# Optimization experiments

Hardware: AMD Instinct MI355X
Metric: run time of the kernel (lower is better)

Reference implementation:

```python
import jax, jax.numpy as jnp
import numpy as np

HEADS = 8
OUT_CH = 128
DIMH_V = 16      # out_channels // heads
DIMH_QK = 8      # dim_head_v // 2
DIM = 128        # attention axis length == init dim
QKV_CH = 256     # heads * (dim_head_v + 2*dim_head_qk) == 2*out_channels
F_QR, F_KR, F_SV, F_SVE = 0.3, 0.3, 0.5, 0.3
BN_EPS = 1e-5


def _bn(x, gamma, beta, axes):
    # BatchNorm in training mode: per-channel (axis=1) batch statistics.
    mean = jnp.mean(x, axis=axes, keepdims=True)
    var = jnp.var(x, axis=axes, keepdims=True)
    xhat = (x - mean) * jax.lax.rsqrt(var + BN_EPS)
    shape = [1] * x.ndim
    shape[1] = -1
    return xhat * gamma.reshape(shape) + beta.reshape(shape)


def setup_inputs() -> dict:
    key = jax.random.key(0)
    ks = jax.random.split(key, 3)
    x = jax.random.normal(ks[0], (8, 128, 64, 128), dtype=jnp.float32)
    w_qkv = jax.random.normal(ks[1], (QKV_CH, 128), dtype=jnp.float32) * 0.05
    relative = jax.random.normal(ks[2], (2 * DIMH_V, 2 * DIM - 1), dtype=jnp.float32) * np.sqrt(1.0 / DIMH_V)
    ones = lambda c: jnp.ones((c,), jnp.float32)
    zeros = lambda c: jnp.zeros((c,), jnp.float32)
    return {
        "x": x, "w_qkv": w_qkv,
        "g1": ones(QKV_CH), "b1": zeros(QKV_CH),
        "g2": ones(QKV_CH), "b2": zeros(QKV_CH),
        "gs": ones(3 * HEADS), "bs": zeros(3 * HEADS),
        "go": ones(2 * OUT_CH), "bo": zeros(2 * OUT_CH),
        "relative": relative,
    }


def reference(x, w_qkv, g1, b1, g2, b2, gs, bs, go, bo, relative):
    N, C, Wax, H = x.shape  # flag=True: permute (0,2,1,3)
    xb = jnp.transpose(x, (0, 2, 1, 3)).reshape(N * Wax, C, H)

    # conv1x1 (no bias) + BN, then bn_qkv
    qkv = jnp.einsum('bch,oc->boh', xb, w_qkv)
    qkv = _bn(qkv, g1, b1, (0, 2))
    qkv = _bn(qkv, g2, b2, (0, 2))

    qkv = qkv.reshape(N * Wax, HEADS, 2 * DIMH_V, H)
    q = qkv[:, :, :DIMH_QK]                      # [b,g,8,H]
    k = qkv[:, :, DIMH_QK:2 * DIMH_QK]           # [b,g,8,H]
    v = qkv[:, :, 2 * DIMH_QK:]                  # [b,g,16,H]

    # gather relative embeddings: index[i,j] = i - j + H - 1
    idx = jnp.arange(H)[:, None] - jnp.arange(H)[None, :] + H - 1
    emb = relative[:, idx]                       # [32,H,H]
    q_emb = emb[:DIMH_QK]
    k_emb = emb[DIMH_QK:2 * DIMH_QK]
    v_emb = emb[2 * DIMH_QK:]

    qr = jnp.einsum('bgci,cij->bgij', q, q_emb) * F_QR
    kr = jnp.swapaxes(jnp.einsum('bgci,cij->bgij', k, k_emb), 2, 3) * F_KR
    qk = jnp.einsum('bgci,bgcj->bgij', q, k)

    stacked = jnp.concatenate([qk, qr, kr], axis=1)           # [b,3g,H,H]
    stacked = _bn(stacked, gs, bs, (0, 2, 3))
    stacked = stacked.reshape(N * Wax, 3, HEADS, H, H).sum(axis=1)
    sim = jax.nn.softmax(stacked, axis=3)                     # [b,g,H,H]

    sv = jnp.einsum('bgij,bgcj->bgci', sim, v) * F_SV
    sve = jnp.einsum('bgij,cij->bgci', sim, v_emb) * F_SVE
    so = jnp.concatenate([sv, sve], axis=-1).reshape(N * Wax, 2 * OUT_CH, H)
    so = _bn(so, go, bo, (0, 2))

    out = so.reshape(N, Wax, OUT_CH, 2, H).sum(axis=3)        # [N,W,Cout,H]
    return jnp.transpose(out, (0, 2, 1, 3))                   # flag=True
```

## Files before the change

### kernel.cpp

```cpp
#include <hip/hip_runtime.h>
#include <hip/hip_fp16.h>
#include <math.h>

#define B_TOT 512
#define CQKV  256
#define CIN   128
#define HLEN  128

static constexpr float F_QR = 0.3f, F_KR = 0.3f, F_SV = 0.5f, F_SVE = 0.3f;
static constexpr float EPS = 1e-5f;

typedef __attribute__((ext_vector_type(8))) short short8v;
typedef __attribute__((ext_vector_type(8))) _Float16 half8v;
typedef __attribute__((ext_vector_type(2))) _Float16 half2v;
typedef __attribute__((ext_vector_type(4))) float float4v;

#if __has_builtin(__builtin_amdgcn_fdot2)
#define HAVE_FDOT2 1
#endif

__device__ __forceinline__ unsigned short f2bf(float f) {
    unsigned u = __float_as_uint(f);
    unsigned r = u + 0x7fffu + ((u >> 16) & 1u);
    return (unsigned short)(r >> 16);
}
__device__ __forceinline__ unsigned short f2h(float f) {
    return __half_as_ushort(__float2half(f));
}

__global__ __launch_bounds__(256, 3) void k_qkv(const float* __restrict__ x,
                                                const float* __restrict__ w,
                                                float* __restrict__ qkv,
                                                double* __restrict__ accA) {
    __shared__ unsigned short As[64][136];
    __shared__ unsigned short Xs[256][64];
    __shared__ float wsum[64][2];
    int bid = blockIdx.x;
    int n   = bid >> 7;
    int sub = bid & 127;
    int mt  = sub >> 2;
    int ot  = sub & 3;
    int m0  = mt << 8;
    int o0  = ot << 6;
    int t   = threadIdx.x;

    if (t < 64) { wsum[t][0] = 0.f; wsum[t][1] = 0.f; }

#pragma unroll
    for (int it = 0; it < 8; ++it) {
        int idx = it * 256 + t;
        int o = idx >> 5, c4 = (idx & 31) << 2;
        float4 wv = *(const float4*)(w + (size_t)(o0 + o) * CIN + c4);
        As[o][c4 + 0] = f2bf(wv.x);
        As[o][c4 + 1] = f2bf(wv.y);
        As[o][c4 + 2] = f2bf(wv.z);
        As[o][c4 + 3] = f2bf(wv.w);
    }

    const float* xn = x + (size_t)n * CIN * 8192 + m0;

    int wv_ = t >> 6, l = t & 63;
    int lr = l & 15, lh = l >> 4;
    int mw = wv_ << 6;

    float4v acc[4][4];
#pragma unroll
    for (int a = 0; a < 4; ++a)
#pragma unroll
        for (int b2 = 0; b2 < 4; ++b2) acc[a][b2] = (float4v){0.f, 0.f, 0.f, 0.f};

    for (int s = 0; s < 2; ++s) {
        int c0 = s << 6;
        __syncthreads();
#pragma unroll
        for (int it = 0; it < 16; ++it) {
            int c  = (it << 2) + (t >> 6);
            int m4 = (t & 63) << 2;
            float4 xv = *(const float4*)(xn + (size_t)(c0 + c) * 8192 + m4);
            float vals[4] = {xv.x, xv.y, xv.z, xv.w};
#pragma unroll
            for (int j = 0; j < 4; ++j) {
                int m = m4 + j;
                int cs = (((c >> 3) ^ ((m >> 2) & 7)) << 3) | (c & 7);
                Xs[m][cs] = f2bf(vals[j]);
            }
        }
        __syncthreads();
#pragma unroll
        for (int ks = 0; ks < 2; ++ks) {
            short8v af[4], bf[4];
#pragma unroll
            for (int a = 0; a < 4; ++a)
                af[a] = *(const short8v*)&As[a * 16 + lr][c0 + ks * 32 + lh * 8];
#pragma unroll
            for (int b2 = 0; b2 < 4; ++b2) {
                int m  = mw + b2 * 16 + lr;
                int cb = (ks * 4 + lh) ^ ((m >> 2) & 7);
                bf[b2] = *(const short8v*)&Xs[m][cb << 3];
            }
#pragma unroll
            for (int a = 0; a < 4; ++a)
#pragma unroll
                for (int b2 = 0; b2 < 4; ++b2)
                    acc[a][b2] = __builtin_amdgcn_mfma_f32_16x16x32_bf16(
                        af[a], bf[b2], acc[a][b2], 0, 0, 0);
        }
    }

#pragma unroll
    for (int a = 0; a < 4; ++a) {
#pragma unroll
        for (int b2 = 0; b2 < 4; ++b2) {
            int m  = m0 + mw + b2 * 16 + lr;
            int bb = n * 64 + (m >> 7);
            int h  = m & 127;
#pragma unroll
            for (int r = 0; r < 4; ++r) {
                int o = o0 + a * 16 + lh * 4 + r;
                qkv[((size_t)bb * CQKV + o) * HLEN + h] = acc[a][b2][r];
            }
        }
    }

#pragma unroll
    for (int a = 0; a < 4; ++a) {
#pragma unroll
        for (int r = 0; r < 4; ++r) {
            float s = 0.f, ss = 0.f;
#pragma unroll
            for (int b2 = 0; b2 < 4; ++b2) {
                float v = acc[a][b2][r];
                s += v; ss += v * v;
            }
#pragma unroll
            for (int off = 1; off < 16; off <<= 1) {
                s  += __shfl_xor(s, off);
                ss += __shfl_xor(ss, off);
            }
            if (lr == 0) {
                int ol = a * 16 + lh * 4 + r;
                atomicAdd(&wsum[ol][0], s);
                atomicAdd(&wsum[ol][1], ss);
            }
        }
    }
    __syncthreads();
    if (t < 64) {
        atomicAdd(&accA[(size_t)(o0 + t) * 2 + 0], (double)wsum[t][0]);
        atomicAdd(&accA[(size_t)(o0 + t) * 2 + 1], (double)wsum[t][1]);
    }
}

__global__ void k_finA(const double* __restrict__ accA,
                       const float* __restrict__ g1, const float* __restrict__ g2,
                       const float* __restrict__ b2,
                       float* __restrict__ scaleA, float* __restrict__ shiftA) {
    int o = threadIdx.x;
    double cnt  = 65536.0;
    double mean = accA[o * 2] / cnt;
    double var  = accA[o * 2 + 1] / cnt - mean * mean;
    float r1 = rsqrtf((float)var + EPS);
    float v2 = g1[o] * g1[o] * (float)var * r1 * r1;
    float sc = g1[o] * g2[o] * r1 * rsqrtf(v2 + EPS);
    scaleA[o] = sc;
    shiftA[o] = b2[o] - (float)mean * sc;
}

__global__ void k_finF(const double* __restrict__ accF,
                       const float* __restrict__ go, const float* __restrict__ bo,
                       float* __restrict__ scaleF, float* __restrict__ shiftF) {
    int o = threadIdx.x;
    double cnt  = 65536.0;
    double mean = accF[o * 2] / cnt;
    double var  = accF[o * 2 + 1] / cnt - mean * mean;
    float sc = go[o] * rsqrtf((float)var + EPS);
    scaleF[o] = sc;
    shiftF[o] = bo[o] - (float)mean * sc;
}

__global__ __launch_bounds__(128) void k_tables(const float* __restrict__ rel,
                                                float* __restrict__ Rq, float* __restrict__ Rk,
                                                float* __restrict__ TqT, float* __restrict__ TkT) {
    int bid = blockIdx.x;
    int i = threadIdx.x;
    int p = bid & 63;
    int c = p >> 3, c2 = p & 7;
    const float* ra = (bid < 64) ? (rel + c * 255)  : (rel + (8 + c) * 255);
    const float* rb = (bid < 64) ? (rel + c2 * 255) : (rel + (8 + c2) * 255);
    float tacc = 0.f;
    for (int kk = 0; kk < 128; ++kk) tacc = fmaf(ra[i + kk], rb[i + kk], tacc);
    if (bid < 64) TqT[i * 64 + p] = tacc; else TkT[i * 64 + p] = tacc;
    if (c2 == 0) {
        float racc = 0.f;
        for (int kk = 0; kk < 128; ++kk) racc += ra[i + kk];
        if (bid < 64) Rq[c * 128 + i] = racc; else Rk[c * 128 + i] = racc;
    }
}

__global__ __launch_bounds__(256) void k_gram(const float* __restrict__ qkv,
                                              const float* __restrict__ scaleA,
                                              const float* __restrict__ shiftA,
                                              const float* __restrict__ Rq,
                                              const float* __restrict__ Rk,
                                              const float* __restrict__ TqT,
                                              const float* __restrict__ TkT,
                                              double* __restrict__ accS) {
    __shared__ float qs[8][132], ks[8][132];
    __shared__ float redA[4][64][4];
    __shared__ float redB[2][18];
    __shared__ float redC[3];
    int blk = blockIdx.x, b = blk >> 3, g = blk & 7;
    int t = threadIdx.x;
    for (int idx = t; idx < 2048; idx += 256) {
        int cc = idx >> 7, h = idx & 127, o = g * 32 + cc;
        float v = qkv[((size_t)b * CQKV + o) * HLEN + h] * scaleA[o] + shiftA[o];
        if (cc < 8) qs[cc][h] = v; else ks[cc - 8][h] = v;
    }
    __syncthreads();
    int lane = t & 63, wv = t >> 6;
    int c = lane >> 3, c2 = lane & 7;
    float gq = 0, gk = 0, tq = 0, tk = 0;
#pragma unroll 4
    for (int ii = 0; ii < 32; ++ii) {
        int i = wv * 32 + ii;
        float a = qs[c][i] * qs[c2][i];
        float e = ks[c][i] * ks[c2][i];
        gq += a; gk += e;
        tq = fmaf(a, TqT[i * 64 + lane], tq);
        tk = fmaf(e, TkT[i * 64 + lane], tk);
    }
    redA[wv][lane][0] = gq; redA[wv][lane][1] = gk;
    redA[wv][lane][2] = tq; redA[wv][lane][3] = tk;

    if (t < 128) {
        int h = t;
        float sqr = 0, skr = 0;
        float sq8l[8], sk8l[8];
#pragma unroll
        for (int c3 = 0; c3 < 8; ++c3) {
            float q0 = qs[c3][h], k0 = ks[c3][h];
            sq8l[c3] = q0; sk8l[c3] = k0;
            sqr = fmaf(q0, Rq[c3 * 128 + h], sqr);
            skr = fmaf(k0, Rk[c3 * 128 + h], skr);
        }
#pragma unroll
        for (int off = 1; off < 64; off <<= 1) {
            sqr += __shfl_xor(sqr, off);
            skr += __shfl_xor(skr, off);
#pragma unroll
            for (int c3 = 0; c3 < 8; ++c3) {
                sq8l[c3] += __shfl_xor(sq8l[c3], off);
                sk8l[c3] += __shfl_xor(sk8l[c3], off);
            }
        }
        if (lane == 0) {
            redB[wv][0] = sqr; redB[wv][1] = skr;
#pragma unroll
            for (int c3 = 0; c3 < 8; ++c3) {
                redB[wv][2 + c3]  = sq8l[c3];
                redB[wv][10 + c3] = sk8l[c3];
            }
        }
    }
    __syncthreads();
    if (t < 64) {
        float Gq = redA[0][t][0] + redA[1][t][0] + redA[2][t][0] + redA[3][t][0];
        float Gk = redA[0][t][1] + redA[1][t][1] + redA[2][t][1] + redA[3][t][1];
        float Tq = redA[0][t][2] + redA[1][t][2] + redA[2][t][2] + redA[3][t][2];
        float Tk = redA[0][t][3] + redA[1][t][3] + redA[2][t][3] + redA[3][t][3];
        float ssqk = Gq * Gk;
#pragma unroll
        for (int off = 1; off < 64; off <<= 1) {
            ssqk += __shfl_xor(ssqk, off);
            Tq   += __shfl_xor(Tq, off);
            Tk   += __shfl_xor(Tk, off);
        }
        if (t == 0) { redC[0] = ssqk; redC[1] = Tq; redC[2] = Tk; }
    }
    __syncthreads();
    if (t == 0) {
        float sqr = redB[0][0] + redB[1][0];
        float skr = redB[0][1] + redB[1][1];
        float sqk = 0;
#pragma unroll
        for (int c3 = 0; c3 < 8; ++c3)
            sqk += (redB[0][2 + c3] + redB[1][2 + c3]) * (redB[0][10 + c3] + redB[1][10 + c3]);
        atomicAdd(&accS[g * 2 + 0], (double)sqk);
        atomicAdd(&accS[g * 2 + 1], (double)redC[0]);
        atomicAdd(&accS[(8 + g) * 2 + 0], (double)(F_QR * sqr));
        atomicAdd(&accS[(8 + g) * 2 + 1], (double)(F_QR * F_QR * redC[1]));
        atomicAdd(&accS[(16 + g) * 2 + 0], (double)(F_KR * skr));
        atomicAdd(&accS[(16 + g) * 2 + 1], (double)(F_KR * F_KR * redC[2]));
    }
}

__global__ void k_sfin(const double* __restrict__ accS,
                       const float* __restrict__ gs, const float* __restrict__ bs,
                       float* __restrict__ scaleS, float* __restrict__ shiftS) {
    int c = threadIdx.x;
    if (c < 24) {
        double cnt  = 512.0 * 128.0 * 128.0;
        double mean = accS[c * 2] / cnt;
        double var  = accS[c * 2 + 1] / cnt - mean * mean;
        float sc = gs[c] * rsqrtf((float)var + EPS);
        scaleS[c] = sc;
        shiftS[c] = bs[c] - (float)mean * sc;
    }
}

__global__ __launch_bounds__(256, 2) void k_attn(const float* __restrict__ qkv,
                                                 const float* __restrict__ scaleA,
                                                 const float* __restrict__ shiftA,
                                                 const float* __restrict__ rel,
                                                 const float* __restrict__ scaleS,
                                                 const float* __restrict__ shiftS,
                                                 float* __restrict__ so,
                                                 double* __restrict__ accF) {
    __shared__ unsigned short qT[128][8];
    __shared__ unsigned short kF[128][8];
    __shared__ unsigned short vB[16][136];
    __shared__ unsigned short rqT[255][8];
    __shared__ unsigned short rkT[255][8];
    __shared__ unsigned short rvA[255][8];
    __shared__ unsigned short rvB[255][8];
    __shared__ unsigned short Pl[128][136];
    __shared__ float accL[32][2];
    int blk = blockIdx.x, b = blk >> 3, g = blk & 7;
    int t = threadIdx.x;
    if (t < 32) { accL[t][0] = 0.f; accL[t][1] = 0.f; }

#pragma unroll
    for (int it = 0; it < 4; ++it) {
        int idx = it * 256 + t;
        int cc = idx >> 5;
        int h4 = (idx & 31) << 2;
        int o = g * 32 + cc;
        float4 v4 = *(const float4*)(qkv + ((size_t)b * CQKV + o) * HLEN + h4);
        float sc = scaleA[o], sh = shiftA[o];
        float f0 = fmaf(v4.x, sc, sh), f1 = fmaf(v4.y, sc, sh);
        float f2 = fmaf(v4.z, sc, sh), f3 = fmaf(v4.w, sc, sh);
        if (cc < 8) {
            qT[h4][cc] = f2h(f0); qT[h4 + 1][cc] = f2h(f1);
            qT[h4 + 2][cc] = f2h(f2); qT[h4 + 3][cc] = f2h(f3);
        } else if (cc < 16) {
            kF[h4][cc - 8] = f2h(f0); kF[h4 + 1][cc - 8] = f2h(f1);
            kF[h4 + 2][cc - 8] = f2h(f2); kF[h4 + 3][cc - 8] = f2h(f3);
        } else {
            uint2 pk;
            pk.x = (unsigned)f2h(f0) | ((unsigned)f2h(f1) << 16);
            pk.y = (unsigned)f2h(f2) | ((unsigned)f2h(f3) << 16);
            *(uint2*)&vB[cc - 16][h4] = pk;
        }
    }
#pragma unroll
    for (int it = 0; it < 8; ++it) {
        int idx = it * 256 + t;
        if (idx < 2040) {
            float4 v = *(const float4*)(rel + (size_t)idx * 4);
            float vv[4] = {v.x, v.y, v.z, v.w};
#pragma unroll
            for (int e = 0; e < 4; ++e) {
                int lin = idx * 4 + e;
                int r = lin / 255;
                int d = lin - r * 255;
                unsigned short us = f2h(vv[e]);
                if (r < 8)       rqT[d][r] = us;
                else if (r < 16) rkT[d][r - 8] = us;
                else if (r < 24) rvA[d][r - 16] = us;
                else             rvB[d][r - 24] = us;
            }
        }
    }
    __syncthreads();

    float cA = scaleS[g], cB = F_QR * scaleS[8 + g], cC = F_KR * scaleS[16 + g];
    float shsum = shiftS[g] + shiftS[8 + g] + shiftS[16 + g];

    int i = t >> 1, j0 = (t & 1) << 6;
    half2v q2[4];
    {
        uint4 qv = *(const uint4*)&qT[i][0];
        q2[0] = *(half2v*)&qv.x; q2[1] = *(half2v*)&qv.y;
        q2[2] = *(half2v*)&qv.z; q2[3] = *(half2v*)&qv.w;
    }

    float p[64];
    float rowmax = -1e30f;
#pragma unroll
    for (int jj = 0; jj < 64; ++jj) {
        int j = j0 + jj;
        uint4 kv = *(const uint4*)&kF[j][0];
        uint4 rq = *(const uint4*)&rqT[i - j + 127][0];
        uint4 rk = *(const uint4*)&rkT[j - i + 127][0];
        half2v* k2p  = (half2v*)&kv;
        half2v* rq2p = (half2v*)&rq;
        half2v* rk2p = (half2v*)&rk;
#ifdef HAVE_FDOT2
        float qk = __builtin_amdgcn_fdot2(q2[0], k2p[0],
                   __builtin_amdgcn_fdot2(q2[1], k2p[1],
                   __builtin_amdgcn_fdot2(q2[2], k2p[2],
                   __builtin_amdgcn_fdot2(q2[3], k2p[3], 0.f, false), false), false), false);
        float qr = __builtin_amdgcn_fdot2(q2[0], rq2p[0],
                   __builtin_amdgcn_fdot2(q2[1], rq2p[1],
                   __builtin_amdgcn_fdot2(q2[2], rq2p[2],
                   __builtin_amdgcn_fdot2(q2[3], rq2p[3], 0.f, false), false), false), false);
        float kr = __builtin_amdgcn_fdot2(k2p[0], rk2p[0],
                   __builtin_amdgcn_fdot2(k2p[1], rk2p[1],
                   __builtin_amdgcn_fdot2(k2p[2], rk2p[2],
                   __builtin_amdgcn_fdot2(k2p[3], rk2p[3], 0.f, false), false), false), false);
#else
        __half2* k2  = (__half2*)&kv;
        __half2* rq2 = (__half2*)&rq;
        __half2* rk2 = (__half2*)&rk;
        __half2* qh2 = (__half2*)&q2[0];
        __half2 hqk = __hfma2(qh2[0], k2[0], __hfma2(qh2[1], k2[1],
                      __hfma2(qh2[2], k2[2], __hmul2(qh2[3], k2[3]))));
        __half2 hqr = __hfma2(qh2[0], rq2[0], __hfma2(qh2[1], rq2[1],
                      __hfma2(qh2[2], rq2[2], __hmul2(qh2[3], rq2[3]))));
        __half2 hkr = __hfma2(k2[0], rk2[0], __hfma2(k2[1], rk2[1],
                      __hfma2(k2[2], rk2[2], __hmul2(k2[3], rk2[3]))));
        float qk = __low2float(hqk) + __high2float(hqk);
        float qr = __low2float(hqr) + __high2float(hqr);
        float kr = __low2float(hkr) + __high2float(hkr);
#endif
        float s = fmaf(qk, cA, fmaf(qr, cB, fmaf(kr, cC, shsum)));
        p[jj] = s;
        rowmax = fmaxf(rowmax, s);
    }
    rowmax = fmaxf(rowmax, __shfl_xor(rowmax, 1));
    float rsum = 0.f;
#pragma unroll
    for (int jj = 0; jj < 64; ++jj) {
        float e = __expf(p[jj] - rowmax);
        p[jj] = e;
        rsum += e;
    }
    rsum += __shfl_xor(rsum, 1);
    float rn = 1.f / rsum;

#pragma unroll
    for (int k8 = 0; k8 < 8; ++k8) {
        uint4 w4;
        unsigned* wp = (unsigned*)&w4;
#pragma unroll
        for (int e = 0; e < 4; ++e) {
            __half2 h2 = __floats2half2_rn(p[8 * k8 + 2 * e] * rn,
                                           p[8 * k8 + 2 * e + 1] * rn);
            wp[e] = *(unsigned*)&h2;
        }
        *(uint4*)&Pl[i][j0 + 8 * k8] = w4;
    }

    __half2 acc2[8];
#pragma unroll
    for (int m = 0; m < 8; ++m) acc2[m] = __floats2half2_rn(0.f, 0.f);
#pragma unroll
    for (int jj = 0; jj < 64; ++jj) {
        int j = j0 + jj;
        int d = i - j + 127;
        __half2 p2 = __float2half2_rn(p[jj]);
        uint4 ra = *(const uint4*)&rvA[d][0];
        uint4 rb = *(const uint4*)&rvB[d][0];
        __half2* ra2 = (__half2*)&ra;
        __half2* rb2 = (__half2*)&rb;
        acc2[0] = __hfma2(p2, ra2[0], acc2[0]);
        acc2[1] = __hfma2(p2, ra2[1], acc2[1]);
        acc2[2] = __hfma2(p2, ra2[2], acc2[2]);
        acc2[3] = __hfma2(p2, ra2[3], acc2[3]);
        acc2[4] = __hfma2(p2, rb2[0], acc2[4]);
        acc2[5] = __hfma2(p2, rb2[1], acc2[5]);
        acc2[6] = __hfma2(p2, rb2[2], acc2[6]);
        acc2[7] = __hfma2(p2, rb2[3], acc2[7]);
    }
    float a1[16];
#pragma unroll
    for (int m = 0; m < 8; ++m) {
        a1[2 * m]     = __low2float(acc2[m]);
        a1[2 * m + 1] = __high2float(acc2[m]);
    }
#pragma unroll
    for (int c = 0; c < 16; ++c) a1[c] += __shfl_xor(a1[c], 1);
    {
        int cbase = (t & 1) * 8;
        float sce = F_SVE * rn;
        float* sop = so + ((size_t)b * CQKV + g * 32) * HLEN + i;
        float svp[8], ssvp[8];
#pragma unroll
        for (int c8 = 0; c8 < 8; ++c8) {
            int c = cbase + c8;
            float v = a1[c] * sce;
            sop[(size_t)(2 * c + 1) * HLEN] = v;
            svp[c8] = v; ssvp[c8] = v * v;
        }
#pragma unroll
        for (int off = 2; off < 64; off <<= 1) {
#pragma unroll
            for (int c8 = 0; c8 < 8; ++c8) {
                svp[c8]  += __shfl_xor(svp[c8], off);
                ssvp[c8] += __shfl_xor(ssvp[c8], off);
            }
        }
        if ((t & 62) == 0) {
#pragma unroll
            for (int c8 = 0; c8 < 8; ++c8) {
                int c = cbase + c8;
                atomicAdd(&accL[2 * c + 1][0], svp[c8]);
                atomicAdd(&accL[2 * c + 1][1], ssvp[c8]);
            }
        }
    }

    __syncthreads();

    {
        int w = t >> 6, l = t & 63;
        int lr = l & 15, lh = l >> 4;
        float s0 = 0.f, ss0 = 0.f;
#pragma unroll
        for (int it = 0; it < 2; ++it) {
            int itile = w * 2 + it;
            float4v acc = {0.f, 0.f, 0.f, 0.f};
#pragma unroll
            for (int ks = 0; ks < 4; ++ks) {
                half8v af = *(const half8v*)&Pl[itile * 16 + lr][ks * 32 + lh * 8];
                half8v bf = *(const half8v*)&vB[lr][ks * 32 + lh * 8];
                acc = __builtin_amdgcn_mfma_f32_16x16x32_f16(af, bf, acc, 0, 0, 0);
            }
            int oc = g * 32 + 2 * lr;
            float* sop = so + ((size_t)b * CQKV + oc) * HLEN + itile * 16 + lh * 4;
            float4 outv;
            outv.x = acc[0] * F_SV; outv.y = acc[1] * F_SV;
            outv.z = acc[2] * F_SV; outv.w = acc[3] * F_SV;
            *(float4*)sop = outv;
            s0  += outv.x + outv.y + outv.z + outv.w;
            ss0 += outv.x * outv.x + outv.y * outv.y + outv.z * outv.z + outv.w * outv.w;
        }
        s0  += __shfl_xor(s0, 16);  s0  += __shfl_xor(s0, 32);
        ss0 += __shfl_xor(ss0, 16); ss0 += __shfl_xor(ss0, 32);
        if (lh == 0) {
            atomicAdd(&accL[2 * lr][0], s0);
            atomicAdd(&accL[2 * lr][1], ss0);
        }
    }
    __syncthreads();
    if (t < 32) {
        int o = g * 32 + t;
        atomicAdd(&accF[(size_t)o * 2 + 0], (double)accL[t][0]);
        atomicAdd(&accF[(size_t)o * 2 + 1], (double)accL[t][1]);
    }
}

__global__ __launch_bounds__(256) void k_out(const float* __restrict__ so,
                                             const float* __restrict__ scale,
                                             const float* __restrict__ shift,
                                             float* __restrict__ out) {
    int b = blockIdx.x, n = b >> 6, wi = b & 63;
    int t = threadIdx.x;
    int h4  = (t & 31) << 2;
    int oc0 = (t >> 5) << 4;
    for (int k = 0; k < 16; ++k) {
        int oc = oc0 + k;
        float4 v0 = *(const float4*)(so + ((size_t)b * CQKV + 2 * oc) * HLEN + h4);
        float4 v1 = *(const float4*)(so + ((size_t)b * CQKV + 2 * oc + 1) * HLEN + h4);
        float s0 = scale[2 * oc], f0 = shift[2 * oc];
        float s1 = scale[2 * oc + 1], f1 = shift[2 * oc + 1];
        float4 o4;
        o4.x = fmaf(v0.x, s0, f0) + fmaf(v1.x, s1, f1);
        o4.y = fmaf(v0.y, s0, f0) + fmaf(v1.y, s1, f1);
        o4.z = fmaf(v0.z, s0, f0) + fmaf(v1.z, s1, f1);
        o4.w = fmaf(v0.w, s0, f0) + fmaf(v1.w, s1, f1);
        *(float4*)(out + (((size_t)n * 128 + oc) * 64 + wi) * HLEN + h4) = o4;
    }
}

extern "C" void kernel_launch(void* const* d_in, const int* in_sizes, int n_in,
                              void* d_out, int out_size, void* d_ws, size_t ws_size,
                              hipStream_t stream) {
    const float* x   = (const float*)d_in[0];
    const float* w   = (const float*)d_in[1];
    const float* g1  = (const float*)d_in[2];
    const float* b1  = (const float*)d_in[3];
    const float* g2  = (const float*)d_in[4];
    const float* b2  = (const float*)d_in[5];
    const float* gs  = (const float*)d_in[6];
    const float* bs  = (const float*)d_in[7];
    const float* go  = (const float*)d_in[8];
    const float* bo  = (const float*)d_in[9];
    const float* rel = (const float*)d_in[10];
    float* out = (float*)d_out;

    float*  qkv    = (float*)d_ws;
    float*  so     = qkv + (size_t)16777216;
    double* accA   = (double*)(so + (size_t)16777216);
    double* accS   = accA + 512;
    double* accF   = accS + 48;
    float*  scaleA = (float*)(accF + 512);
    float*  shiftA = scaleA + 256;
    float*  scaleS = shiftA + 256;
    float*  shiftS = scaleS + 24;
    float*  scaleF = shiftS + 24;
    float*  shiftF = scaleF + 256;
    float*  Rq     = shiftF + 256;
    float*  Rk     = Rq + 1024;
    float*  TqT    = Rk + 1024;
    float*  TkT    = TqT + 8192;

    hipMemsetAsync(accA, 0, (512 + 48 + 512) * sizeof(double), stream);

    k_qkv<<<1024, 256, 0, stream>>>(x, w, qkv, accA);
    k_tables<<<128, 128, 0, stream>>>(rel, Rq, Rk, TqT, TkT);
    k_finA<<<1, 256, 0, stream>>>(accA, g1, g2, b2, scaleA, shiftA);
    k_gram<<<4096, 256, 0, stream>>>(qkv, scaleA, shiftA, Rq, Rk, TqT, TkT, accS);
    k_sfin<<<1, 32, 0, stream>>>(accS, gs, bs, scaleS, shiftS);
    k_attn<<<4096, 256, 0, stream>>>(qkv, scaleA, shiftA, rel, scaleS, shiftS, so, accF);
    k_finF<<<1, 256, 0, stream>>>(accF, go, bo, scaleF, shiftF);
    k_out<<<512, 256, 0, stream>>>(so, scaleF, shiftF, out);
}
```

Before: 344.9 us.

## Compute attention scores directly in MFMA operand layout, drop shared P buffer

Remaps the thread-to-(i,j) assignment so each lane computes the score elements it later feeds as the MFMA A-operand. The softmax probabilities therefore stay in registers instead of being staged through a 34KB shared buffer. This removes the LDS writes and reads and the block barrier for P. Launch bounds rise from 2 to 4 blocks per CU to exploit the lower LDS use. The risk is register pressure and spilling under the tighter bound, plus the row reductions now need cross-lane shuffles over 16/32 offsets. The sve accumulation reduction is now done in half precision, which may reduce accuracy slightly.

```diff
diff --git a/kernel.cpp b/kernel.cpp
--- a/kernel.cpp
+++ b/kernel.cpp
@@ -308,7 +308,7 @@
     }
 }
 
-__global__ __launch_bounds__(256, 2) void k_attn(const float* __restrict__ qkv,
+__global__ __launch_bounds__(256, 4) void k_attn(const float* __restrict__ qkv,
                                                  const float* __restrict__ scaleA,
                                                  const float* __restrict__ shiftA,
                                                  const float* __restrict__ rel,
@@ -323,7 +323,6 @@
     __shared__ unsigned short rkT[255][8];
     __shared__ unsigned short rvA[255][8];
     __shared__ unsigned short rvB[255][8];
-    __shared__ unsigned short Pl[128][136];
     __shared__ float accL[32][2];
     int blk = blockIdx.x, b = blk >> 3, g = blk & 7;
     int t = threadIdx.x;
@@ -376,153 +375,199 @@
     float cA = scaleS[g], cB = F_QR * scaleS[8 + g], cC = F_KR * scaleS[16 + g];
     float shsum = shiftS[g] + shiftS[8 + g] + shiftS[16 + g];
 
-    int i = t >> 1, j0 = (t & 1) << 6;
-    half2v q2[4];
+    int w = t >> 6, l = t & 63;
+    int lr = l & 15, lh = l >> 4;
+    int i0 = w * 32 + lr;
+
+    half2v q2[2][4];
     {
-        uint4 qv = *(const uint4*)&qT[i][0];
-        q2[0] = *(half2v*)&qv.x; q2[1] = *(half2v*)&qv.y;
-        q2[2] = *(half2v*)&qv.z; q2[3] = *(half2v*)&qv.w;
-    }
-
-    float p[64];
-    float rowmax = -1e30f;
-#pragma unroll
-    for (int jj = 0; jj < 64; ++jj) {
-        int j = j0 + jj;
-        uint4 kv = *(const uint4*)&kF[j][0];
-        uint4 rq = *(const uint4*)&rqT[i - j + 127][0];
-        uint4 rk = *(const uint4*)&rkT[j - i + 127][0];
-        half2v* k2p  = (half2v*)&kv;
-        half2v* rq2p = (half2v*)&rq;
-        half2v* rk2p = (half2v*)&rk;
+        uint4 qv0 = *(const uint4*)&qT[i0][0];
+        uint4 qv1 = *(const uint4*)&qT[i0 + 16][0];
+        q2[0][0] = *(half2v*)&qv0.x; q2[0][1] = *(half2v*)&qv0.y;
+        q2[0][2] = *(half2v*)&qv0.z; q2[0][3] = *(half2v*)&qv0.w;
+        q2[1][0] = *(half2v*)&qv1.x; q2[1][1] = *(half2v*)&qv1.y;
+        q2[1][2] = *(half2v*)&qv1.z; q2[1][3] = *(half2v*)&qv1.w;
+    }
+
+    float p0[32], p1[32];
+    float rm0 = -1e30f, rm1 = -1e30f;
+#pragma unroll
+    for (int ks = 0; ks < 4; ++ks) {
+#pragma unroll
+        for (int e = 0; e < 8; ++e) {
+            int j = ks * 32 + lh * 8 + e;
+            uint4 kv = *(const uint4*)&kF[j][0];
+            half2v* k2p = (half2v*)&kv;
+#pragma unroll
+            for (int it2 = 0; it2 < 2; ++it2) {
+                int i = i0 + it2 * 16;
+                uint4 rq = *(const uint4*)&rqT[i - j + 127][0];
+                uint4 rk = *(const uint4*)&rkT[j - i + 127][0];
+                half2v* rq2p = (half2v*)&rq;
+                half2v* rk2p = (half2v*)&rk;
 #ifdef HAVE_FDOT2
-        float qk = __builtin_amdgcn_fdot2(q2[0], k2p[0],
-                   __builtin_amdgcn_fdot2(q2[1], k2p[1],
-                   __builtin_amdgcn_fdot2(q2[2], k2p[2],
-                   __builtin_amdgcn_fdot2(q2[3], k2p[3], 0.f, false), false), false), false);
-        float qr = __builtin_amdgcn_fdot2(q2[0], rq2p[0],
-                   __builtin_amdgcn_fdot2(q2[1], rq2p[1],
-                   __builtin_amdgcn_fdot2(q2[2], rq2p[2],
-                   __builtin_amdgcn_fdot2(q2[3], rq2p[3], 0.f, false), false), false), false);
-        float kr = __builtin_amdgcn_fdot2(k2p[0], rk2p[0],
-                   __builtin_amdgcn_fdot2(k2p[1], rk2p[1],
-                   __builtin_amdgcn_fdot2(k2p[2], rk2p[2],
-                   __builtin_amdgcn_fdot2(k2p[3], rk2p[3], 0.f, false), false), false), false);
+                float qk = __builtin_amdgcn_fdot2(q2[it2][0], k2p[0],
+                           __builtin_amdgcn_fdot2(q2[it2][1], k2p[1],
+                           __builtin_amdgcn_fdot2(q2[it2][2], k2p[2],
+                           __builtin_amdgcn_fdot2(q2[it2][3], k2p[3], 0.f, false), false), false), false);
+                float qr = __builtin_amdgcn_fdot2(q2[it2][0], rq2p[0],
+                           __builtin_amdgcn_fdot2(q2[it2][1], rq2p[1],
+                           __builtin_amdgcn_fdot2(q2[it2][2], rq2p[2],
+                           __builtin_amdgcn_fdot2(q2[it2][3], rq2p[3], 0.f, false), false), false), false);
+                float kr = __builtin_amdgcn_fdot2(k2p[0], rk2p[0],
+                           __builtin_amdgcn_fdot2(k2p[1], rk2p[1],
+                           __builtin_amdgcn_fdot2(k2p[2], rk2p[2],
+                           __builtin_amdgcn_fdot2(k2p[3], rk2p[3], 0.f, false), false), false), false);
 #else
-        __half2* k2  = (__half2*)&kv;
-        __half2* rq2 = (__half2*)&rq;
-        __half2* rk2 = (__half2*)&rk;
-        __half2* qh2 = (__half2*)&q2[0];
-        __half2 hqk = __hfma2(qh2[0], k2[0], __hfma2(qh2[1], k2[1],
-                      __hfma2(qh2[2], k2[2], __hmul2(qh2[3], k2[3]))));
-        __half2 hqr = __hfma2(qh2[0], rq2[0], __hfma2(qh2[1], rq2[1],
-                      __hfma2(qh2[2], rq2[2], __hmul2(qh2[3], rq2[3]))));
-        __half2 hkr = __hfma2(k2[0], rk2[0], __hfma2(k2[1], rk2[1],
-                      __hfma2(k2[2], rk2[2], __hmul2(k2[3], rk2[3]))));
-        float qk = __low2float(hqk) + __high2float(hqk);
-        float qr = __low2float(hqr) + __high2float(hqr);
-        float kr = __low2float(hkr) + __high2float(hkr);
+                __half2* qh = (__half2*)&q2[it2][0];
+                __half2* kk2 = (__half2*)&kv;
+                __half2* rq2 = (__half2*)&rq;
+                __half2* rk2 = (__half2*)&rk;
+                __half2 hqk = __hfma2(qh[0], kk2[0], __hfma2(qh[1], kk2[1],
+                              __hfma2(qh[2], kk2[2], __hmul2(qh[3], kk2[3]))));
+                __half2 hqr = __hfma2(qh[0], rq2[0], __hfma2(qh[1], rq2[1],
+                              __hfma2(qh[2], rq2[2], __hmul2(qh[3], rq2[3]))));
+                __half2 hkr = __hfma2(kk2[0], rk2[0], __hfma2(kk2[1], rk2[1],
+                              __hfma2(kk2[2], rk2[2], __hmul2(kk2[3], rk2[3]))));
+                float qk = __low2float(hqk) + __high2float(hqk);
+                float qr = __low2float(hqr) + __high2float(hqr);
+                float kr = __low2float(hkr) + __high2float(hkr);
 #endif
-        float s = fmaf(qk, cA, fmaf(qr, cB, fmaf(kr, cC, shsum)));
-        p[jj] = s;
-        rowmax = fmaxf(rowmax, s);
-    }
-    rowmax = fmaxf(rowmax, __shfl_xor(rowmax, 1));
-    float rsum = 0.f;
-#pragma unroll
-    for (int jj = 0; jj < 64; ++jj) {
-        float e = __expf(p[jj] - rowmax);
-        p[jj] = e;
-        rsum += e;
-    }
-    rsum += __shfl_xor(rsum, 1);
-    float rn = 1.f / rsum;
-
-#pragma unroll
-    for (int k8 = 0; k8 < 8; ++k8) {
-        uint4 w4;
-        unsigned* wp = (unsigned*)&w4;
-#pragma unroll
-        for (int e = 0; e < 4; ++e) {
-            __half2 h2 = __floats2half2_rn(p[8 * k8 + 2 * e] * rn,
-                                           p[8 * k8 + 2 * e + 1] * rn);
-            wp[e] = *(unsigned*)&h2;
-        }
-        *(uint4*)&Pl[i][j0 + 8 * k8] = w4;
-    }
-
-    __half2 acc2[8];
-#pragma unroll
-    for (int m = 0; m < 8; ++m) acc2[m] = __floats2half2_rn(0.f, 0.f);
-#pragma unroll
-    for (int jj = 0; jj < 64; ++jj) {
-        int j = j0 + jj;
-        int d = i - j + 127;
-        __half2 p2 = __float2half2_rn(p[jj]);
-        uint4 ra = *(const uint4*)&rvA[d][0];
-        uint4 rb = *(const uint4*)&rvB[d][0];
-        __half2* ra2 = (__half2*)&ra;
-        __half2* rb2 = (__half2*)&rb;
-        acc2[0] = __hfma2(p2, ra2[0], acc2[0]);
-        acc2[1] = __hfma2(p2, ra2[1], acc2[1]);
-        acc2[2] = __hfma2(p2, ra2[2], acc2[2]);
-        acc2[3] = __hfma2(p2, ra2[3], acc2[3]);
-        acc2[4] = __hfma2(p2, rb2[0], acc2[4]);
-        acc2[5] = __hfma2(p2, rb2[1], acc2[5]);
-        acc2[6] = __hfma2(p2, rb2[2], acc2[6]);
-        acc2[7] = __hfma2(p2, rb2[3], acc2[7]);
-    }
-    float a1[16];
+                float s = fmaf(qk, cA, fmaf(qr, cB, fmaf(kr, cC, shsum)));
+                if (it2 == 0) { p0[ks * 8 + e] = s; rm0 = fmaxf(rm0, s); }
+                else          { p1[ks * 8 + e] = s; rm1 = fmaxf(rm1, s); }
+            }
+        }
+    }
+    rm0 = fmaxf(rm0, __shfl_xor(rm0, 16)); rm0 = fmaxf(rm0, __shfl_xor(rm0, 32));
+    rm1 = fmaxf(rm1, __shfl_xor(rm1, 16)); rm1 = fmaxf(rm1, __shfl_xor(rm1, 32));
+    float rs0 = 0.f, rs1 = 0.f;
+#pragma unroll
+    for (int kk = 0; kk < 32; ++kk) {
+        p0[kk] = __expf(p0[kk] - rm0); rs0 += p0[kk];
+        p1[kk] = __expf(p1[kk] - rm1); rs1 += p1[kk];
+    }
+    rs0 += __shfl_xor(rs0, 16); rs0 += __shfl_xor(rs0, 32);
+    rs1 += __shfl_xor(rs1, 16); rs1 += __shfl_xor(rs1, 32);
+    float rn0 = 1.f / rs0, rn1 = 1.f / rs1;
+
+    __half2 accA2[8], accB2[8];
 #pragma unroll
     for (int m = 0; m < 8; ++m) {
-        a1[2 * m]     = __low2float(acc2[m]);
-        a1[2 * m + 1] = __high2float(acc2[m]);
-    }
-#pragma unroll
-    for (int c = 0; c < 16; ++c) a1[c] += __shfl_xor(a1[c], 1);
+        accA2[m] = __floats2half2_rn(0.f, 0.f);
+        accB2[m] = __floats2half2_rn(0.f, 0.f);
+    }
+#pragma unroll
+    for (int ks = 0; ks < 4; ++ks) {
+#pragma unroll
+        for (int e = 0; e < 8; ++e) {
+            int j = ks * 32 + lh * 8 + e;
+            {
+                int d = i0 - j + 127;
+                __half2 p2 = __float2half2_rn(p0[ks * 8 + e]);
+                uint4 ra = *(const uint4*)&rvA[d][0];
+                uint4 rb = *(const uint4*)&rvB[d][0];
+                __half2* ra2 = (__half2*)&ra;
+                __half2* rb2 = (__half2*)&rb;
+                accA2[0] = __hfma2(p2, ra2[0], accA2[0]);
+                accA2[1] = __hfma2(p2, ra2[1], accA2[1]);
+                accA2[2] = __hfma2(p2, ra2[2], accA2[2]);
+                accA2[3] = __hfma2(p2, ra2[3], accA2[3]);
+                accA2[4] = __hfma2(p2, rb2[0], accA2[4]);
+                accA2[5] = __hfma2(p2, rb2[1], accA2[5]);
+                accA2[6] = __hfma2(p2, rb2[2], accA2[6]);
+                accA2[7] = __hfma2(p2, rb2[3], accA2[7]);
+            }
+            {
+                int d = i0 + 16 - j + 127;
+                __half2 p2 = __float2half2_rn(p1[ks * 8 + e]);
+                uint4 ra = *(const uint4*)&rvA[d][0];
+                uint4 rb = *(const uint4*)&rvB[d][0];
+                __half2* ra2 = (__half2*)&ra;
+                __half2* rb2 = (__half2*)&rb;
+                accB2[0] = __hfma2(p2, ra2[0], accB2[0]);
+                accB2[1] = __hfma2(p2, ra2[1], accB2[1]);
+                accB2[2] = __hfma2(p2, ra2[2], accB2[2]);
+                accB2[3] = __hfma2(p2, ra2[3], accB2[3]);
+                accB2[4] = __hfma2(p2, rb2[0], accB2[4]);
+                accB2[5] = __hfma2(p2, rb2[1], accB2[5]);
+                accB2[6] = __hfma2(p2, rb2[2], accB2[6]);
+                accB2[7] = __hfma2(p2, rb2[3], accB2[7]);
+            }
+        }
+    }
+#pragma unroll
+    for (int m = 0; m < 8; ++m) {
+        unsigned ua = *(unsigned*)&accA2[m];
+        unsigned t1 = __shfl_xor(ua, 16);
+        accA2[m] = __hadd2(accA2[m], *(__half2*)&t1);
+        ua = *(unsigned*)&accA2[m];
+        t1 = __shfl_xor(ua, 32);
+        accA2[m] = __hadd2(accA2[m], *(__half2*)&t1);
+        unsigned ub = *(unsigned*)&accB2[m];
+        unsigned t2 = __shfl_xor(ub, 16);
+        accB2[m] = __hadd2(accB2[m], *(__half2*)&t2);
+        ub = *(unsigned*)&accB2[m];
+        t2 = __shfl_xor(ub, 32);
+        accB2[m] = __hadd2(accB2[m], *(__half2*)&t2);
+    }
     {
-        int cbase = (t & 1) * 8;
-        float sce = F_SVE * rn;
-        float* sop = so + ((size_t)b * CQKV + g * 32) * HLEN + i;
-        float svp[8], ssvp[8];
-#pragma unroll
-        for (int c8 = 0; c8 < 8; ++c8) {
-            int c = cbase + c8;
-            float v = a1[c] * sce;
-            sop[(size_t)(2 * c + 1) * HLEN] = v;
-            svp[c8] = v; ssvp[c8] = v * v;
-        }
-#pragma unroll
-        for (int off = 2; off < 64; off <<= 1) {
-#pragma unroll
-            for (int c8 = 0; c8 < 8; ++c8) {
-                svp[c8]  += __shfl_xor(svp[c8], off);
-                ssvp[c8] += __shfl_xor(ssvp[c8], off);
-            }
-        }
-        if ((t & 62) == 0) {
-#pragma unroll
-            for (int c8 = 0; c8 < 8; ++c8) {
-                int c = cbase + c8;
-                atomicAdd(&accL[2 * c + 1][0], svp[c8]);
-                atomicAdd(&accL[2 * c + 1][1], ssvp[c8]);
-            }
-        }
-    }
-
-    __syncthreads();
+        float sce0 = F_SVE * rn0, sce1 = F_SVE * rn1;
+        float s_c[4], ss_c[4];
+#pragma unroll
+        for (int cc = 0; cc < 4; ++cc) {
+            int c = lh * 4 + cc;
+            __half2 ha = accA2[c >> 1];
+            __half2 hb = accB2[c >> 1];
+            float v0 = ((c & 1) ? __high2float(ha) : __low2float(ha)) * sce0;
+            float v1 = ((c & 1) ? __high2float(hb) : __low2float(hb)) * sce1;
+            size_t base = ((size_t)b * CQKV + g * 32 + 2 * c + 1) * HLEN;
+            so[base + i0]      = v0;
+            so[base + i0 + 16] = v1;
+            s_c[cc]  = v0 + v1;
+            ss_c[cc] = v0 * v0 + v1 * v1;
+        }
+#pragma unroll
+        for (int off = 1; off < 16; off <<= 1) {
+#pragma unroll
+            for (int cc = 0; cc < 4; ++cc) {
+                s_c[cc]  += __shfl_xor(s_c[cc], off);
+                ss_c[cc] += __shfl_xor(ss_c[cc], off);
+            }
+        }
+        if (lr == 0) {
+#pragma unroll
+            for (int cc = 0; cc < 4; ++cc) {
+                int c = lh * 4 + cc;
+                atomicAdd(&accL[2 * c + 1][0], s_c[cc]);
+                atomicAdd(&accL[2 * c + 1][1], ss_c[cc]);
+            }
+        }
+    }
+
+    unsigned ph[32];
+#pragma unroll
+    for (int ks = 0; ks < 4; ++ks) {
+#pragma unroll
+        for (int e2 = 0; e2 < 4; ++e2) {
+            __half2 h0 = __floats2half2_rn(p0[ks * 8 + 2 * e2] * rn0,
+                                           p0[ks * 8 + 2 * e2 + 1] * rn0);
+            __half2 h1 = __floats2half2_rn(p1[ks * 8 + 2 * e2] * rn1,
+                                           p1[ks * 8 + 2 * e2 + 1] * rn1);
+            ph[ks * 4 + e2]      = *(unsigned*)&h0;
+            ph[16 + ks * 4 + e2] = *(unsigned*)&h1;
+        }
+    }
 
     {
-        int w = t >> 6, l = t & 63;
-        int lr = l & 15, lh = l >> 4;
         float s0 = 0.f, ss0 = 0.f;
 #pragma unroll
-        for (int it = 0; it < 2; ++it) {
-            int itile = w * 2 + it;
+        for (int it2 = 0; it2 < 2; ++it2) {
+            int itile = w * 2 + it2;
             float4v acc = {0.f, 0.f, 0.f, 0.f};
 #pragma unroll
             for (int ks = 0; ks < 4; ++ks) {
-                half8v af = *(const half8v*)&Pl[itile * 16 + lr][ks * 32 + lh * 8];
+                half8v af = *(half8v*)&ph[it2 * 16 + ks * 4];
                 half8v bf = *(const half8v*)&vB[lr][ks * 32 + lh * 8];
                 acc = __builtin_amdgcn_mfma_f32_16x16x32_f16(af, bf, acc, 0, 0, 0);
             }
```

New measurement: 313.4 us. 9.1% less time.
